# Optimization experiments

Measured on AMD Instinct MI355X. Metric: run time of the kernel, lower is better.

The kernel has to match this reference:

```python
import jax, jax.numpy as jnp
import numpy as np

N = 50000      # nodes
E = 800000     # edges (avg degree 16)
IN = 128       # in_channels
OUT = 128      # out_channels
H1, C1 = 4, 64 # conv1: 4 heads x 64 -> concat 256
H2, C2 = 1, OUT
NEG_SLOPE = 0.2


def setup_inputs() -> dict:
    key = jax.random.key(0)
    ks = jax.random.split(key, 10)
    def glorot(k, shape, fan):
        return jax.random.normal(k, shape, jnp.float32) * (1.0 / np.sqrt(fan))
    x = jax.random.normal(ks[0], (N, IN), jnp.float32)
    edge_index = jax.random.randint(ks[1], (2, E), 0, N)
    W1 = glorot(ks[2], (IN, H1 * C1), IN)
    att_src1 = glorot(ks[3], (H1, C1), C1)
    att_dst1 = glorot(ks[4], (H1, C1), C1)
    b1 = jnp.zeros((H1 * C1,), jnp.float32)
    W2 = glorot(ks[5], (H1 * C1, H2 * C2), H1 * C1)
    att_src2 = glorot(ks[6], (H2, C2), C2)
    att_dst2 = glorot(ks[7], (H2, C2), C2)
    b2 = jnp.zeros((OUT,), jnp.float32)
    return {"x": x, "edge_index": edge_index,
            "W1": W1, "att_src1": att_src1, "att_dst1": att_dst1, "b1": b1,
            "W2": W2, "att_src2": att_src2, "att_dst2": att_dst2, "b2": b2}


def gat_conv(x, src, dst, W, att_s, att_d, bias, heads, ch):
    """PyG GATConv: linear -> edge attention -> per-dst softmax -> scatter-sum."""
    n = x.shape[0]
    h = (x @ W).reshape(n, heads, ch)                      # [N, H, C]
    a_s = jnp.einsum('nhc,hc->nh', h, att_s)               # [N, H]
    a_d = jnp.einsum('nhc,hc->nh', h, att_d)               # [N, H]
    e = jax.nn.leaky_relu(a_s[src] + a_d[dst], NEG_SLOPE)  # [Etot, H]
    e_max = jax.ops.segment_max(e, dst, num_segments=n)    # [N, H]
    e = jnp.exp(e - e_max[dst])
    denom = jax.ops.segment_sum(e, dst, num_segments=n)    # [N, H]
    alpha = e / (denom[dst] + 1e-16)                        # [Etot, H]
    msg = h[src] * alpha[:, :, None]                        # [Etot, H, C]
    out = jax.ops.segment_sum(msg, dst, num_segments=n)     # [N, H, C]
    return out.reshape(n, heads * ch) + bias


def reference(x, edge_index, W1, att_src1, att_dst1, b1, W2, att_src2, att_dst2, b2):
    n = x.shape[0]
    loop = jnp.arange(n)
    # GATConv(add_self_loops=True): append (i, i) edges
    src = jnp.concatenate([edge_index[0], loop])
    dst = jnp.concatenate([edge_index[1], loop])
    h = jax.nn.relu(gat_conv(x, src, dst, W1, att_src1, att_dst1, b1, H1, C1))
    out = jax.nn.relu(gat_conv(h, src, dst, W2, att_src2, att_dst2, b2, H2, C2))
    return out
```

## Files before the change

### kernel.cpp

```cpp
#include <hip/hip_runtime.h>
#include <hip/hip_bf16.h>
#include <hip/hip_fp16.h>


#define NEG_SLOPE 0.2f

typedef __attribute__((ext_vector_type(8))) _Float16 f16x8;
typedef __attribute__((ext_vector_type(8))) short s16x8;
typedef __attribute__((ext_vector_type(4))) float f32x4;

__device__ inline void loadH8(float* v, const __half* p) {
    union { s16x8 raw; __half2 h2[4]; } u;
    u.raw = *(const s16x8*)p;
#pragma unroll
    for (int i = 0; i < 4; ++i) {
        float2 f = __half22float2(u.h2[i]);
        v[2 * i] = f.x;
        v[2 * i + 1] = f.y;
    }
}

__device__ inline f16x8 loadAfrag(const __half* __restrict__ p) {
    return *(const f16x8*)p;
}
__device__ inline f16x8 loadAfrag(const float* __restrict__ p) {
    float4 a = *(const float4*)p;
    float4 b = *(const float4*)(p + 4);
    union { f16x8 v; __half hv[8]; } u;
    u.hv[0] = __float2half(a.x); u.hv[1] = __float2half(a.y);
    u.hv[2] = __float2half(a.z); u.hv[3] = __float2half(a.w);
    u.hv[4] = __float2half(b.x); u.hv[5] = __float2half(b.y);
    u.hv[6] = __float2half(b.z); u.hv[7] = __float2half(b.w);
    return u.v;
}


template<int K, int NN, int H, bool ATOMIC, typename AT>
__device__ void gemm_body(int bx, int M,
        const AT* __restrict__ A, const float* __restrict__ W,
        const float* __restrict__ att_s, const float* __restrict__ att_d,
        float* __restrict__ as_, float* __restrict__ ad_,
        __half* __restrict__ Hout) {
    constexpr int KS = K >> 5;
    constexpr int CW = NN / 64;
    constexpr int RW = 4 / CW;
    constexpr int C = NN / H;
    const int lane = threadIdx.x & 63;
    const int w = threadIdx.x >> 6;
    const int wr = w / CW;
    const int wc = w % CW;
    const int quad = lane >> 4;
    const int r16 = lane & 15;
    const int mBase = bx * (RW * 32) + wr * 32;
    const int nBase = wc * 64;
    const int head = nBase / C;

    f32x4 acc[2][4];
#pragma unroll
    for (int rt = 0; rt < 2; ++rt)
#pragma unroll
        for (int ct = 0; ct < 4; ++ct) acc[rt][ct] = (f32x4){0.f, 0.f, 0.f, 0.f};

#pragma unroll
    for (int ks = 0; ks < KS; ++ks) {
        f16x8 af[2];
#pragma unroll
        for (int rt = 0; rt < 2; ++rt) {
            int row = mBase + rt * 16 + r16;
            if (row < M) {
                af[rt] = loadAfrag(A + (size_t)row * K + ks * 32 + quad * 8);
            } else {
                af[rt] = (f16x8){0, 0, 0, 0, 0, 0, 0, 0};
            }
        }
        f16x8 bf[4];
#pragma unroll
        for (int ct = 0; ct < 4; ++ct) {
            int k0 = ks * 32 + quad * 8;
            int n0 = nBase + ct * 16 + r16;
            union { f16x8 v; __half hv[8]; } u;
#pragma unroll
            for (int j = 0; j < 8; ++j)
                u.hv[j] = __float2half(W[(size_t)(k0 + j) * NN + n0]);
            bf[ct] = u.v;
        }
#pragma unroll
        for (int rt = 0; rt < 2; ++rt)
#pragma unroll
            for (int ct = 0; ct < 4; ++ct)
                acc[rt][ct] = __builtin_amdgcn_mfma_f32_16x16x32_f16(af[rt], bf[ct], acc[rt][ct], 0, 0, 0);
    }

#pragma unroll
    for (int rt = 0; rt < 2; ++rt)
#pragma unroll
        for (int ct = 0; ct < 4; ++ct) {
            int row0 = mBase + rt * 16 + quad * 4;
            int col = nBase + ct * 16 + r16;
#pragma unroll
            for (int r = 0; r < 4; ++r) {
                int row = row0 + r;
                if (row < M) Hout[(size_t)row * NN + col] = __float2half(acc[rt][ct][r]);
            }
        }

    float attS[4], attD[4];
#pragma unroll
    for (int ct = 0; ct < 4; ++ct) {
        int cc = (nBase % C) + ct * 16 + r16;
        attS[ct] = att_s[head * C + cc];
        attD[ct] = att_d[head * C + cc];
    }
#pragma unroll
    for (int rt = 0; rt < 2; ++rt)
#pragma unroll
        for (int r = 0; r < 4; ++r) {
            float ps = 0.f, pd = 0.f;
#pragma unroll
            for (int ct = 0; ct < 4; ++ct) {
                ps += acc[rt][ct][r] * attS[ct];
                pd += acc[rt][ct][r] * attD[ct];
            }
#pragma unroll
            for (int off = 1; off < 16; off <<= 1) {
                ps += __shfl_xor(ps, off);
                pd += __shfl_xor(pd, off);
            }
            int row = mBase + rt * 16 + quad * 4 + r;
            if (r16 == 0 && row < M) {
                if (ATOMIC) {
                    atomicAdd(&as_[row * H + head], ps);
                    atomicAdd(&ad_[row * H + head], pd);
                } else {
                    as_[row * H + head] = ps;
                    ad_[row * H + head] = pd;
                }
            }
        }
}


__global__ __launch_bounds__(256) void gemm1_scatter(
        int EPB, const int* __restrict__ ei, int E, int N,
        int* __restrict__ cnt, int* __restrict__ csr_src,
        const float* __restrict__ x, const float* __restrict__ W1,
        const float* __restrict__ att_s, const float* __restrict__ att_d,
        float* __restrict__ as_, float* __restrict__ ad_,
        __half* __restrict__ Hout) {
    const int Etot = E + N;
    int e0 = blockIdx.x * EPB;
    int e1 = e0 + EPB; if (e1 > Etot) e1 = Etot;
    for (int e = e0 + (int)threadIdx.x; e < e1; e += 256) {
        int s, d;
        if (e < E) { s = ei[e]; d = ei[E + e]; } else { s = e - E; d = s; }
        int r = atomicAdd(&cnt[d], 1);
        if (r < 64) csr_src[(d << 6) + r] = s;
    }
    gemm_body<128, 256, 4, false, float>(blockIdx.x, N, x, W1,
                                         att_s, att_d, as_, ad_, Hout);
}

__global__ __launch_bounds__(256) void gemm2_kernel(
        int M, const __half* __restrict__ A, const float* __restrict__ W2,
        const float* __restrict__ att_s, const float* __restrict__ att_d,
        float* __restrict__ as_, float* __restrict__ ad_,
        __half* __restrict__ Hout) {
    gemm_body<256, 128, 1, true, __half>(blockIdx.x, M, A, W2,
                                         att_s, att_d, as_, ad_, Hout);
}


__device__ inline float edge_w(float a) {
    float e = a > 0.f ? a : NEG_SLOPE * a;
    return __expf(e);
}

template<int U, int HC, int H, int GRP>
__device__ inline void agg_step(int p, const int* __restrict__ csr_src,
                                const __half* __restrict__ h,
                                const float* __restrict__ as_, float adv,
                                int c0, int head, float* acc, float& den) {
    int srcv[U];
#pragma unroll
    for (int u = 0; u < U; ++u) srcv[u] = csr_src[p + u * GRP];
    float f[U][8];
#pragma unroll
    for (int u = 0; u < U; ++u) loadH8(f[u], h + (size_t)srcv[u] * HC + c0);
    float wv[U];
#pragma unroll
    for (int u = 0; u < U; ++u) wv[u] = edge_w(as_[srcv[u] * H + head] + adv);
#pragma unroll
    for (int u = 0; u < U; ++u) den += wv[u];
#pragma unroll
    for (int u = 0; u < U; ++u)
#pragma unroll
        for (int i = 0; i < 8; ++i) acc[i] += wv[u] * f[u][i];
}

template<int HC, int H, bool F16OUT>
__global__ __launch_bounds__(256) void fused_agg(int N,
                                                 const int* __restrict__ cnt,
                                                 const int* __restrict__ csr_src,
                                                 const __half* __restrict__ h,
                                                 const float* __restrict__ as_,
                                                 const float* __restrict__ ad_,
                                                 const float* __restrict__ bias,
                                                 float* __restrict__ out,
                                                 __half* __restrict__ outh) {
    constexpr int LPE = HC / 8;
    constexpr int GRP = 64 / LPE;
    constexpr int C = HC / H;
    const int n = blockIdx.x * 4 + (threadIdx.x >> 6);
    if (n >= N) return;
    const int lane = threadIdx.x & 63;
    const int g = lane / LPE;
    const int lq = lane % LPE;
    const int c0 = lq * 8;
    const int head = c0 / C;
    const int s0 = n << 6;
    int deg = cnt[n]; if (deg > 64) deg = 64;
    const int s1 = s0 + deg;
    const float adv = ad_[n * H + head];
    float acc[8] = {};
    float den = 0.f;
    int p = s0 + g;
    for (; p + 3 * GRP < s1; p += 4 * GRP)
        agg_step<4, HC, H, GRP>(p, csr_src, h, as_, adv, c0, head, acc, den);
    for (; p < s1; p += GRP)
        agg_step<1, HC, H, GRP>(p, csr_src, h, as_, adv, c0, head, acc, den);
#pragma unroll
    for (int off = LPE; off < 64; off <<= 1) {
        den += __shfl_xor(den, off);
#pragma unroll
        for (int i = 0; i < 8; ++i) acc[i] += __shfl_xor(acc[i], off);
    }
    if (g == 0) {
        float dinv = 1.0f / (den + 1e-16f);
        float o[8];
#pragma unroll
        for (int i = 0; i < 8; ++i) {
            float v = acc[i] * dinv + bias[c0 + i];
            o[i] = v > 0.f ? v : 0.f;
        }
        if (F16OUT) {
            union { s16x8 raw; __half hv[8]; } u;
#pragma unroll
            for (int i = 0; i < 8; ++i) u.hv[i] = __float2half(o[i]);
            *(s16x8*)(outh + (size_t)n * HC + c0) = u.raw;
        } else {
            float4 v0 = make_float4(o[0], o[1], o[2], o[3]);
            float4 v1 = make_float4(o[4], o[5], o[6], o[7]);
            *(float4*)(out + (size_t)n * HC + c0) = v0;
            *(float4*)(out + (size_t)n * HC + c0 + 4) = v1;
        }
    }
}

extern "C" void kernel_launch(void* const* d_in, const int* in_sizes, int n_in,
                              void* d_out, int out_size, void* d_ws, size_t ws_size,
                              hipStream_t stream) {
    const float* x      = (const float*)d_in[0];
    const int*   ei     = (const int*)d_in[1];
    const float* W1     = (const float*)d_in[2];
    const float* att_s1 = (const float*)d_in[3];
    const float* att_d1 = (const float*)d_in[4];
    const float* b1     = (const float*)d_in[5];
    const float* W2     = (const float*)d_in[6];
    const float* att_s2 = (const float*)d_in[7];
    const float* att_d2 = (const float*)d_in[8];
    const float* b2     = (const float*)d_in[9];
    float* out = (float*)d_out;

    const int N_ = in_sizes[0] / 128;
    const int E_ = in_sizes[1] / 2;
    const int Etot = E_ + N_;

    __half* h1 = (__half*)d_ws;
    __half* x2 = h1 + (size_t)N_ * 256;
    float* as1 = (float*)(x2 + (size_t)N_ * 256);
    float* ad1 = as1 + (size_t)N_ * 4;
    int*   cnt = (int*)(ad1 + (size_t)N_ * 4);
    float* as2 = (float*)(cnt + N_);
    float* ad2 = as2 + N_;
    size_t zeroBytes = (size_t)(3 * N_) * 4;
    int* csr_src = (int*)(ad2 + N_);

    int G1B = (N_ + 31) / 32;
    int G2B = (N_ + 63) / 64;
    int EPB = (Etot + G1B - 1) / G1B;

    hipMemsetAsync(cnt, 0, zeroBytes, stream);

    gemm1_scatter<<<G1B, 256, 0, stream>>>(
        EPB, ei, E_, N_, cnt, csr_src, x, W1, att_s1, att_d1, as1, ad1, h1);
    fused_agg<256, 4, true><<<(N_ + 3) / 4, 256, 0, stream>>>(
        N_, cnt, csr_src, h1, as1, ad1, b1, nullptr, x2);

    __half* h2 = h1;
    gemm2_kernel<<<G2B, 256, 0, stream>>>(
        N_, x2, W2, att_s2, att_d2, as2, ad2, h2);
    fused_agg<128, 1, false><<<(N_ + 3) / 4, 256, 0, stream>>>(
        N_, cnt, csr_src, h2, as2, ad2, b2, out, nullptr);

    (void)n_in; (void)out_size; (void)ws_size;
}
```

Measured before the change: 275.0 us.

## Prepack weights into MFMA fragment layout and split scatter into separate blocks

Adds a prep kernel that converts W1 and W2 to fp16 in the exact per-lane MFMA B-fragment order and zeroes the counters, replacing the hipMemsetAsync. Each GEMM wave then reads one 16-byte vector per fragment instead of eight strided fp32 loads with conversions. The edge scatter into CSR now runs in its own dedicated blocks, one edge per thread, ahead of the GEMM blocks in the same launch, rather than being looped inside every GEMM block. In exchange there is an extra small kernel launch and a workspace layout change.

```diff
diff --git a/kernel.cpp b/kernel.cpp
--- a/kernel.cpp
+++ b/kernel.cpp
@@ -35,9 +35,30 @@
 }
 
 
+__device__ inline void pack_w_elem(const float* __restrict__ W, __half* __restrict__ bp,
+                                   int K, int N, int tid) {
+    int k = tid / N, n = tid - k * N;
+    int ks = k >> 5, k5 = k & 31, quad = k5 >> 3, j = k5 & 7;
+    int ct = n >> 4;
+    int lane = quad * 16 + (n & 15);
+    size_t idx = ((size_t)(ct * (K >> 5) + ks) * 64 + lane) * 8 + j;
+    bp[idx] = __float2half(W[tid]);
+}
+
+__global__ __launch_bounds__(256) void pack_prep(
+        const float* __restrict__ W1, __half* __restrict__ bp1,
+        const float* __restrict__ W2, __half* __restrict__ bp2,
+        int* __restrict__ zp, int zn) {
+    int tid = blockIdx.x * blockDim.x + threadIdx.x;
+    if (tid < 128 * 256) pack_w_elem(W1, bp1, 128, 256, tid);
+    if (tid < 256 * 128) pack_w_elem(W2, bp2, 256, 128, tid);
+    for (int i = tid; i < zn; i += 32768) zp[i] = 0;
+}
+
+
 template<int K, int NN, int H, bool ATOMIC, typename AT>
 __device__ void gemm_body(int bx, int M,
-        const AT* __restrict__ A, const float* __restrict__ W,
+        const AT* __restrict__ A, const __half* __restrict__ Bp,
         const float* __restrict__ att_s, const float* __restrict__ att_d,
         float* __restrict__ as_, float* __restrict__ ad_,
         __half* __restrict__ Hout) {
@@ -76,13 +97,9 @@
         f16x8 bf[4];
 #pragma unroll
         for (int ct = 0; ct < 4; ++ct) {
-            int k0 = ks * 32 + quad * 8;
-            int n0 = nBase + ct * 16 + r16;
-            union { f16x8 v; __half hv[8]; } u;
-#pragma unroll
-            for (int j = 0; j < 8; ++j)
-                u.hv[j] = __float2half(W[(size_t)(k0 + j) * NN + n0]);
-            bf[ct] = u.v;
+            int ctg = (nBase >> 4) + ct;
+            size_t off = ((size_t)(ctg * KS + ks) * 64 + lane) * 8;
+            bf[ct] = *(const f16x8*)(Bp + off);
         }
 #pragma unroll
         for (int rt = 0; rt < 2; ++rt)
@@ -141,31 +158,32 @@
 
 
 __global__ __launch_bounds__(256) void gemm1_scatter(
-        int EPB, const int* __restrict__ ei, int E, int N,
+        int FB, const int* __restrict__ ei, int E, int N,
         int* __restrict__ cnt, int* __restrict__ csr_src,
-        const float* __restrict__ x, const float* __restrict__ W1,
+        const float* __restrict__ x, const __half* __restrict__ Bp,
         const float* __restrict__ att_s, const float* __restrict__ att_d,
         float* __restrict__ as_, float* __restrict__ ad_,
         __half* __restrict__ Hout) {
-    const int Etot = E + N;
-    int e0 = blockIdx.x * EPB;
-    int e1 = e0 + EPB; if (e1 > Etot) e1 = Etot;
-    for (int e = e0 + (int)threadIdx.x; e < e1; e += 256) {
+    if ((int)blockIdx.x < FB) {
+        int e = blockIdx.x * 256 + threadIdx.x;
+        int Etot = E + N;
+        if (e >= Etot) return;
         int s, d;
         if (e < E) { s = ei[e]; d = ei[E + e]; } else { s = e - E; d = s; }
         int r = atomicAdd(&cnt[d], 1);
         if (r < 64) csr_src[(d << 6) + r] = s;
-    }
-    gemm_body<128, 256, 4, false, float>(blockIdx.x, N, x, W1,
+        return;
+    }
+    gemm_body<128, 256, 4, false, float>(blockIdx.x - FB, N, x, Bp,
                                          att_s, att_d, as_, ad_, Hout);
 }
 
 __global__ __launch_bounds__(256) void gemm2_kernel(
-        int M, const __half* __restrict__ A, const float* __restrict__ W2,
+        int M, const __half* __restrict__ A, const __half* __restrict__ Bp,
         const float* __restrict__ att_s, const float* __restrict__ att_d,
         float* __restrict__ as_, float* __restrict__ ad_,
         __half* __restrict__ Hout) {
-    gemm_body<256, 128, 1, true, __half>(blockIdx.x, M, A, W2,
+    gemm_body<256, 128, 1, true, __half>(blockIdx.x, M, A, Bp,
                                          att_s, att_d, as_, ad_, Hout);
 }
 
@@ -277,28 +295,29 @@
 
     __half* h1 = (__half*)d_ws;
     __half* x2 = h1 + (size_t)N_ * 256;
-    float* as1 = (float*)(x2 + (size_t)N_ * 256);
+    __half* bp1 = x2 + (size_t)N_ * 256;
+    __half* bp2 = bp1 + 32768;
+    float* as1 = (float*)(bp2 + 32768);
     float* ad1 = as1 + (size_t)N_ * 4;
     int*   cnt = (int*)(ad1 + (size_t)N_ * 4);
     float* as2 = (float*)(cnt + N_);
     float* ad2 = as2 + N_;
-    size_t zeroBytes = (size_t)(3 * N_) * 4;
     int* csr_src = (int*)(ad2 + N_);
 
+    int FB  = (Etot + 255) / 256;
     int G1B = (N_ + 31) / 32;
     int G2B = (N_ + 63) / 64;
-    int EPB = (Etot + G1B - 1) / G1B;
-
-    hipMemsetAsync(cnt, 0, zeroBytes, stream);
-
-    gemm1_scatter<<<G1B, 256, 0, stream>>>(
-        EPB, ei, E_, N_, cnt, csr_src, x, W1, att_s1, att_d1, as1, ad1, h1);
+
+    pack_prep<<<128, 256, 0, stream>>>(W1, bp1, W2, bp2, cnt, 3 * N_);
+
+    gemm1_scatter<<<FB + G1B, 256, 0, stream>>>(
+        FB, ei, E_, N_, cnt, csr_src, x, bp1, att_s1, att_d1, as1, ad1, h1);
     fused_agg<256, 4, true><<<(N_ + 3) / 4, 256, 0, stream>>>(
         N_, cnt, csr_src, h1, as1, ad1, b1, nullptr, x2);
 
     __half* h2 = h1;
     gemm2_kernel<<<G2B, 256, 0, stream>>>(
-        N_, x2, W2, att_s2, att_d2, as2, ad2, h2);
+        N_, x2, bp2, att_s2, att_d2, as2, ad2, h2);
     fused_agg<128, 1, false><<<(N_ + 3) / 4, 256, 0, stream>>>(
         N_, cnt, csr_src, h2, as2, ad2, b2, out, nullptr);
 
```

Measured after the change: 295.2 us. +7.3%, slower.
